# Performance work log

Hardware: AMD Instinct MI355X
Metric: run time of the kernel (lower is better)

## Reference

```python
import jax, jax.numpy as jnp
import numpy as np

NT = 128
T = 262144


def setup_inputs() -> dict:
    key = jax.random.key(0)
    k1, k2, k3, k4, k5 = jax.random.split(key, 5)
    emit = jax.random.normal(k1, (T, NT), dtype=jnp.float32)
    y = jax.random.randint(k2, (T,), 0, NT, dtype=jnp.int64)
    trans = jax.random.normal(k3, (NT, NT), dtype=jnp.float32)
    strans = jax.random.normal(k4, (NT,), dtype=jnp.float32)
    etrans = jax.random.normal(k5, (NT,), dtype=jnp.float32)
    return {"emit": emit, "y": y, "trans": trans, "strans": strans, "etrans": etrans}


def _crf_nll(emit, y, trans, strans, etrans):
    Tlen = emit.shape[0]

    # forward algorithm (log partition) via scan over timesteps 1..T-1
    alpha0 = strans + emit[0]  # [nt]

    def step(alpha, e_t):
        # alpha_new[n] = logsumexp_p(alpha[p] + trans[p, n]) + emit_t[n]
        alpha_new = jax.nn.logsumexp(alpha[:, None] + trans, axis=0) + e_t
        return alpha_new, None

    alpha, _ = jax.lax.scan(step, alpha0, emit[1:])
    logZ = jax.nn.logsumexp(alpha + etrans)

    # gold score (faithful to original: emissions indexed by the *previous* tag)
    prev = y[:-1]
    nxt = y[1:]
    score = strans[y[0]]
    score = score + jnp.sum(trans[prev, nxt] + emit[jnp.arange(Tlen - 1), prev])
    score = score + etrans[y[-1]] + emit[-1, y[-1]]

    return logZ - score


def reference(emit, y, trans, strans, etrans):
    return _crf_nll(emit, y, trans, strans, etrans)
```

## Files before the change

kernel.cpp:

```cpp
#include <hip/hip_runtime.h>

typedef _Float16 f16x4 __attribute__((ext_vector_type(4)));
typedef float    f32x4 __attribute__((ext_vector_type(4)));

#define T_LEN   262144
#define NTAG    128
#define LCH     64
#define BURN    32
#define NSTEP   96
#define MCH     16
#define NFWD    256
#define NSCORE  256

__global__ __launch_bounds__(256) void crf_fused(
    const float* __restrict__ emit, const int* __restrict__ y,
    const float* __restrict__ trans, const float* __restrict__ strans,
    const float* __restrict__ etrans, double* __restrict__ ws)
{
  if (blockIdx.x >= NFWD) {
    __shared__ float sred[4];
    int idx0 = (blockIdx.x - NFWD) * 256 + threadIdx.x;
    float v = 0.f;
    for (int t = idx0; t < T_LEN - 1; t += NSCORE * 256) {
      int yt = y[t], yn = y[t + 1];
      v += trans[yt * NTAG + yn] + emit[(size_t)t * NTAG + yt];
    }
    if (idx0 == 0) {
      int yl = y[T_LEN - 1];
      v += strans[y[0]] + etrans[yl] + emit[(size_t)(T_LEN - 1) * NTAG + yl];
    }
#pragma unroll
    for (int off = 1; off < 64; off <<= 1) v += __shfl_xor(v, off, 64);
    if ((threadIdx.x & 63) == 0) sred[threadIdx.x >> 6] = v;
    __syncthreads();
    if (threadIdx.x == 0)
      atomicAdd(&ws[1], (double)(sred[0] + sred[1] + sred[2] + sred[3]));
    return;
  }

  __shared__ uint2 pb[8][64];
  __shared__ float emlds[MCH][132];
  __shared__ float wmaxT[MCH][4];

  const int tid   = threadIdx.x;
  const int w     = tid >> 6;
  const int l     = tid & 63;
  const int chunk = l & 15;
  const int grp   = l >> 4;
  const int g0    = blockIdx.x * MCH;
  const int gc    = g0 + chunk;
  const bool lane_g0 = (gc == 0);

  f16x4 qa[2][8];
#pragma unroll
  for (int mt = 0; mt < 2; ++mt) {
    const int out = 32 * w + 16 * mt + chunk;
#pragma unroll
    for (int kt = 0; kt < 8; ++kt) {
      f16x4 a;
#pragma unroll
      for (int j = 0; j < 4; ++j)
        a[j] = (_Float16)__expf(trans[(size_t)(16 * kt + 4 * grp + j) * NTAG + out]);
      qa[mt][kt] = a;
    }
  }

  const int c_row = tid >> 4;
  const int c16   = tid & 15;
  auto erow = [&](int i) -> int {
    int gcr = g0 + c_row;
    return (gcr == 0) ? (i + 1) : (gcr * LCH - BURN + i);
  };

  {
    const float* rp = emit + (size_t)erow(0) * NTAG;
    float4 e0 = *(const float4*)(rp + 4 * c16);
    float4 e1 = *(const float4*)(rp + 4 * c16 + 64);
    *(float4*)&emlds[c_row][4 * c16]      = e0;
    *(float4*)&emlds[c_row][4 * c16 + 64] = e1;
  }

  float b[2][4];
#pragma unroll
  for (int mt = 0; mt < 2; ++mt)
#pragma unroll
    for (int r = 0; r < 4; ++r) b[mt][r] = 0.f;
  if (lane_g0) {
#pragma unroll
    for (int mt = 0; mt < 2; ++mt)
#pragma unroll
      for (int r = 0; r < 4; ++r) {
        int tag = 32 * w + 16 * mt + 4 * grp + r;
        b[mt][r] = strans[tag] + emit[tag];
      }
  }
  float vm = b[0][0];
#pragma unroll
  for (int r = 1; r < 4; ++r) vm = fmaxf(vm, b[0][r]);
#pragma unroll
  for (int r = 0; r < 4; ++r) vm = fmaxf(vm, b[1][r]);
  vm = fmaxf(vm, __shfl_xor(vm, 16, 64));
  vm = fmaxf(vm, __shfl_xor(vm, 32, 64));
  if (grp == 0) wmaxT[chunk][w] = vm;
  __syncthreads();
  float4 wm0 = *(const float4*)&wmaxT[chunk][0];
  float m = fmaxf(fmaxf(wm0.x, wm0.y), fmaxf(wm0.z, wm0.w));
  float acc = lane_g0 ? m : 0.f;
#pragma unroll
  for (int mt = 0; mt < 2; ++mt) {
    union { uint2 u; f16x4 h; } pk;
#pragma unroll
    for (int r = 0; r < 4; ++r) pk.h[r] = (_Float16)__expf(b[mt][r] - m);
    pb[2 * w + mt][l] = pk.u;
  }
  __syncthreads();

  float4 pf0, pf1;
  for (int s = 0; s < NSTEP; ++s) {
    if (s < NSTEP - 1) {
      const float* rp = emit + (size_t)erow(s + 1) * NTAG;
      pf0 = *(const float4*)(rp + 4 * c16);
      pf1 = *(const float4*)(rp + 4 * c16 + 64);
    }
    f32x4 c0 = {0.f, 0.f, 0.f, 0.f};
    f32x4 c1 = {0.f, 0.f, 0.f, 0.f};
#pragma unroll
    for (int kt = 0; kt < 8; ++kt) {
      union { uint2 u; f16x4 h; } bf;
      bf.u = pb[kt][l];
      c0 = __builtin_amdgcn_mfma_f32_16x16x16f16(qa[0][kt], bf.h, c0, 0, 0, 0);
      c1 = __builtin_amdgcn_mfma_f32_16x16x16f16(qa[1][kt], bf.h, c1, 0, 0, 0);
    }
    float4 em0 = *(const float4*)&emlds[chunk][32 * w + 4 * grp];
    float4 em1 = *(const float4*)&emlds[chunk][32 * w + 16 + 4 * grp];
    b[0][0] = __logf(c0[0]) + em0.x;
    b[0][1] = __logf(c0[1]) + em0.y;
    b[0][2] = __logf(c0[2]) + em0.z;
    b[0][3] = __logf(c0[3]) + em0.w;
    b[1][0] = __logf(c1[0]) + em1.x;
    b[1][1] = __logf(c1[1]) + em1.y;
    b[1][2] = __logf(c1[2]) + em1.z;
    b[1][3] = __logf(c1[3]) + em1.w;
    vm = b[0][0];
#pragma unroll
    for (int r = 1; r < 4; ++r) vm = fmaxf(vm, b[0][r]);
#pragma unroll
    for (int r = 0; r < 4; ++r) vm = fmaxf(vm, b[1][r]);
    vm = fmaxf(vm, __shfl_xor(vm, 16, 64));
    vm = fmaxf(vm, __shfl_xor(vm, 32, 64));
    if (grp == 0) wmaxT[chunk][w] = vm;
    __syncthreads();
    float4 wm = *(const float4*)&wmaxT[chunk][0];
    m = fmaxf(fmaxf(wm.x, wm.y), fmaxf(wm.z, wm.w));
    {
      int tstate = lane_g0 ? (s + 1) : (gc * LCH - BURN + s);
      if (tstate >= gc * LCH && tstate < gc * LCH + LCH) acc += m;
    }
    float pf[2][4];
#pragma unroll
    for (int mt = 0; mt < 2; ++mt) {
      union { uint2 u; f16x4 h; } pk;
#pragma unroll
      for (int r = 0; r < 4; ++r) {
        pf[mt][r] = __expf(b[mt][r] - m);
        pk.h[r]   = (_Float16)pf[mt][r];
      }
      pb[2 * w + mt][l] = pk.u;
    }
    if (s == NSTEP - 1 && blockIdx.x == NFWD - 1 && chunk == 15) {
      float lv = 0.f;
#pragma unroll
      for (int mt = 0; mt < 2; ++mt)
#pragma unroll
        for (int r = 0; r < 4; ++r)
          lv += pf[mt][r] * __expf(etrans[32 * w + 16 * mt + 4 * grp + r]);
      atomicAdd(&ws[2], (double)lv);
    }
    if (s < NSTEP - 1) {
      *(float4*)&emlds[c_row][4 * c16]      = pf0;
      *(float4*)&emlds[c_row][4 * c16 + 64] = pf1;
    }
    __syncthreads();
  }

  if (w == 0) {
    float a = acc;
#pragma unroll
    for (int off = 1; off < 16; off <<= 1) a += __shfl_xor(a, off, 64);
    if (l == 0) atomicAdd(&ws[0], (double)a);
  }
}

__global__ void crf_final(const double* __restrict__ ws, float* __restrict__ out)
{
  out[0] = (float)(ws[0] + log(ws[2]) - ws[1]);
}

extern "C" void kernel_launch(void* const* d_in, const int* in_sizes, int n_in,
                              void* d_out, int out_size, void* d_ws, size_t ws_size,
                              hipStream_t stream)
{
  const float* emit   = (const float*)d_in[0];
  const int*   y      = (const int*)d_in[1];
  const float* trans  = (const float*)d_in[2];
  const float* strans = (const float*)d_in[3];
  const float* etrans = (const float*)d_in[4];
  float*  out = (float*)d_out;
  double* ws  = (double*)d_ws;

  hipMemsetAsync(ws, 0, 3 * sizeof(double), stream);
  crf_fused<<<dim3(NFWD + NSCORE), dim3(256), 0, stream>>>(
      emit, y, trans, strans, etrans, ws);
  crf_final<<<dim3(1), dim3(1), 0, stream>>>(ws, out);
}
```

Before: 88.60 us.

## Rewrite forward pass as per-wave chunks with full-tag MFMA and in-kernel finalize

Restructures the chunked forward algorithm so each wave owns 16 chunks and computes all 128 output tags itself with a 8x8 MFMA tile held in registers. It removes the LDS exchange and block-wide barriers of the old per-step loop. Chunks shrink to 16 steps with a 16-step burn-in, so there are many more chunks and blocks. The log/exp is replaced by a scaled-probability recurrence that multiplies by exp(emit) and renormalizes by the max. The final combine now runs via a last-block atomic counter instead of a separate kernel. The trade-offs are much higher register pressure from 64 f16x4 A fragments, double the burn-in overhead ratio, and a shorter warm-up that could affect accuracy.

```diff
diff --git a/kernel.cpp b/kernel.cpp
--- a/kernel.cpp
+++ b/kernel.cpp
@@ -5,23 +5,26 @@
 
 #define T_LEN   262144
 #define NTAG    128
-#define LCH     64
-#define BURN    32
-#define NSTEP   96
-#define MCH     16
-#define NFWD    256
-#define NSCORE  256
+#define LCH     16
+#define BURN    16
+#define NSTEP   (LCH + BURN)
+#define NCHUNK  (T_LEN / LCH)
+#define NWAVE   (NCHUNK / 16)
+#define NSCOREB 256
+#define NFWDB   (NWAVE / 4)
+#define NBLK    (NSCOREB + NFWDB)
 
-__global__ __launch_bounds__(256) void crf_fused(
+__global__ __launch_bounds__(256, 2) void crf_all(
     const float* __restrict__ emit, const int* __restrict__ y,
     const float* __restrict__ trans, const float* __restrict__ strans,
-    const float* __restrict__ etrans, double* __restrict__ ws)
+    const float* __restrict__ etrans, double* __restrict__ ws,
+    float* __restrict__ out)
 {
-  if (blockIdx.x >= NFWD) {
+  if (blockIdx.x < NSCOREB) {
     __shared__ float sred[4];
-    int idx0 = (blockIdx.x - NFWD) * 256 + threadIdx.x;
+    int idx0 = blockIdx.x * 256 + threadIdx.x;
     float v = 0.f;
-    for (int t = idx0; t < T_LEN - 1; t += NSCORE * 256) {
+    for (int t = idx0; t < T_LEN - 1; t += NSCOREB * 256) {
       int yt = y[t], yn = y[t + 1];
       v += trans[yt * NTAG + yn] + emit[(size_t)t * NTAG + yt];
     }
@@ -35,165 +38,146 @@
     __syncthreads();
     if (threadIdx.x == 0)
       atomicAdd(&ws[1], (double)(sred[0] + sred[1] + sred[2] + sred[3]));
-    return;
+  } else {
+    const int w   = threadIdx.x >> 6;
+    const int l   = threadIdx.x & 63;
+    const int col = l & 15;
+    const int grp = l >> 4;
+    const int gw  = (blockIdx.x - NSCOREB) * 4 + w;
+    const int gc  = gw * 16 + col;
+
+    f16x4 a[8][8];
+#pragma unroll
+    for (int rt = 0; rt < 8; ++rt) {
+      const int outtag = 16 * rt + col;
+#pragma unroll
+      for (int kt = 0; kt < 8; ++kt) {
+        f16x4 t4;
+#pragma unroll
+        for (int j = 0; j < 4; ++j)
+          t4[j] = (_Float16)__expf(trans[(16 * kt + 4 * grp + j) * NTAG + outtag]);
+        a[rt][kt] = t4;
+      }
+    }
+
+    f16x4 b[8];
+    float acc = 0.f;
+    if (gc == 0) {
+      float al[8][4];
+      float vm = -1e30f;
+#pragma unroll
+      for (int kt = 0; kt < 8; ++kt)
+#pragma unroll
+        for (int r = 0; r < 4; ++r) {
+          int tag = 16 * kt + 4 * grp + r;
+          al[kt][r] = strans[tag] + emit[tag];
+          vm = fmaxf(vm, al[kt][r]);
+        }
+      vm = fmaxf(vm, __shfl_xor(vm, 16, 64));
+      vm = fmaxf(vm, __shfl_xor(vm, 32, 64));
+      acc = vm;
+#pragma unroll
+      for (int kt = 0; kt < 8; ++kt) {
+        f16x4 nb;
+#pragma unroll
+        for (int r = 0; r < 4; ++r) nb[r] = (_Float16)__expf(al[kt][r] - vm);
+        b[kt] = nb;
+      }
+    } else {
+#pragma unroll
+      for (int kt = 0; kt < 8; ++kt) {
+        f16x4 nb;
+#pragma unroll
+        for (int r = 0; r < 4; ++r) nb[r] = (_Float16)1.0f;
+        b[kt] = nb;
+      }
+    }
+
+    const int row0 = (gc == 0) ? 1 : (gc * LCH - BURN);
+    const float* ebase = emit + (size_t)row0 * NTAG + 4 * grp;
+    float4 pf[8];
+#pragma unroll
+    for (int rt = 0; rt < 8; ++rt) pf[rt] = *(const float4*)(ebase + 16 * rt);
+    ebase += NTAG;
+
+#pragma unroll 1
+    for (int s = 0; s < NSTEP; ++s) {
+      f32x4 c[8];
+#pragma unroll
+      for (int rt = 0; rt < 8; ++rt) c[rt] = (f32x4){0.f, 0.f, 0.f, 0.f};
+#pragma unroll
+      for (int kt = 0; kt < 8; ++kt)
+#pragma unroll
+        for (int rt = 0; rt < 8; ++rt)
+          c[rt] = __builtin_amdgcn_mfma_f32_16x16x16f16(a[rt][kt], b[kt], c[rt], 0, 0, 0);
+
+      float e[8][4];
+#pragma unroll
+      for (int rt = 0; rt < 8; ++rt) {
+        e[rt][0] = __expf(pf[rt].x);
+        e[rt][1] = __expf(pf[rt].y);
+        e[rt][2] = __expf(pf[rt].z);
+        e[rt][3] = __expf(pf[rt].w);
+      }
+      if (s < NSTEP - 1) {
+#pragma unroll
+        for (int rt = 0; rt < 8; ++rt) pf[rt] = *(const float4*)(ebase + 16 * rt);
+        ebase += NTAG;
+      }
+
+      float u[8][4];
+      float vm = -1e30f;
+#pragma unroll
+      for (int rt = 0; rt < 8; ++rt)
+#pragma unroll
+        for (int r = 0; r < 4; ++r) {
+          u[rt][r] = c[rt][r] * e[rt][r];
+          vm = fmaxf(vm, u[rt][r]);
+        }
+      vm = fmaxf(vm, __shfl_xor(vm, 16, 64));
+      vm = fmaxf(vm, __shfl_xor(vm, 32, 64));
+      const float lm   = __logf(vm);
+      const bool  on   = (gc == 0) ? (s <= LCH - 2) : (s >= BURN);
+      if (on) acc += lm;
+      const float rinv = __frcp_rn(vm);
+#pragma unroll
+      for (int kt = 0; kt < 8; ++kt) {
+        f16x4 nb;
+#pragma unroll
+        for (int r = 0; r < 4; ++r) nb[r] = (_Float16)(u[kt][r] * rinv);
+        b[kt] = nb;
+      }
+
+      if (s == NSTEP - 1 && gc == NCHUNK - 1) {
+        float lv = 0.f;
+#pragma unroll
+        for (int rt = 0; rt < 8; ++rt)
+#pragma unroll
+          for (int r = 0; r < 4; ++r)
+            lv += (u[rt][r] * rinv) * __expf(etrans[16 * rt + 4 * grp + r]);
+        lv += __shfl_xor(lv, 16, 64);
+        lv += __shfl_xor(lv, 32, 64);
+        if (grp == 0) atomicAdd(&ws[2], (double)lv);
+      }
+    }
+
+    float av = (grp == 0) ? acc : 0.f;
+#pragma unroll
+    for (int off = 1; off < 64; off <<= 1) av += __shfl_xor(av, off, 64);
+    if (l == 0) atomicAdd(&ws[0], (double)av);
   }
 
-  __shared__ uint2 pb[8][64];
-  __shared__ float emlds[MCH][132];
-  __shared__ float wmaxT[MCH][4];
-
-  const int tid   = threadIdx.x;
-  const int w     = tid >> 6;
-  const int l     = tid & 63;
-  const int chunk = l & 15;
-  const int grp   = l >> 4;
-  const int g0    = blockIdx.x * MCH;
-  const int gc    = g0 + chunk;
-  const bool lane_g0 = (gc == 0);
-
-  f16x4 qa[2][8];
-#pragma unroll
-  for (int mt = 0; mt < 2; ++mt) {
-    const int out = 32 * w + 16 * mt + chunk;
-#pragma unroll
-    for (int kt = 0; kt < 8; ++kt) {
-      f16x4 a;
-#pragma unroll
-      for (int j = 0; j < 4; ++j)
-        a[j] = (_Float16)__expf(trans[(size_t)(16 * kt + 4 * grp + j) * NTAG + out]);
-      qa[mt][kt] = a;
+  __syncthreads();
+  if (threadIdx.x == 0) {
+    __threadfence();
+    unsigned t = atomicAdd((unsigned*)&ws[3], 1u);
+    if (t == NBLK - 1) {
+      double d0 = atomicAdd(&ws[0], 0.0);
+      double d1 = atomicAdd(&ws[1], 0.0);
+      double d2 = atomicAdd(&ws[2], 0.0);
+      out[0] = (float)(d0 + log(d2) - d1);
     }
   }
-
-  const int c_row = tid >> 4;
-  const int c16   = tid & 15;
-  auto erow = [&](int i) -> int {
-    int gcr = g0 + c_row;
-    return (gcr == 0) ? (i + 1) : (gcr * LCH - BURN + i);
-  };
-
-  {
-    const float* rp = emit + (size_t)erow(0) * NTAG;
-    float4 e0 = *(const float4*)(rp + 4 * c16);
-    float4 e1 = *(const float4*)(rp + 4 * c16 + 64);
-    *(float4*)&emlds[c_row][4 * c16]      = e0;
-    *(float4*)&emlds[c_row][4 * c16 + 64] = e1;
-  }
-
-  float b[2][4];
-#pragma unroll
-  for (int mt = 0; mt < 2; ++mt)
-#pragma unroll
-    for (int r = 0; r < 4; ++r) b[mt][r] = 0.f;
-  if (lane_g0) {
-#pragma unroll
-    for (int mt = 0; mt < 2; ++mt)
-#pragma unroll
-      for (int r = 0; r < 4; ++r) {
-        int tag = 32 * w + 16 * mt + 4 * grp + r;
-        b[mt][r] = strans[tag] + emit[tag];
-      }
-  }
-  float vm = b[0][0];
-#pragma unroll
-  for (int r = 1; r < 4; ++r) vm = fmaxf(vm, b[0][r]);
-#pragma unroll
-  for (int r = 0; r < 4; ++r) vm = fmaxf(vm, b[1][r]);
-  vm = fmaxf(vm, __shfl_xor(vm, 16, 64));
-  vm = fmaxf(vm, __shfl_xor(vm, 32, 64));
-  if (grp == 0) wmaxT[chunk][w] = vm;
-  __syncthreads();
-  float4 wm0 = *(const float4*)&wmaxT[chunk][0];
-  float m = fmaxf(fmaxf(wm0.x, wm0.y), fmaxf(wm0.z, wm0.w));
-  float acc = lane_g0 ? m : 0.f;
-#pragma unroll
-  for (int mt = 0; mt < 2; ++mt) {
-    union { uint2 u; f16x4 h; } pk;
-#pragma unroll
-    for (int r = 0; r < 4; ++r) pk.h[r] = (_Float16)__expf(b[mt][r] - m);
-    pb[2 * w + mt][l] = pk.u;
-  }
-  __syncthreads();
-
-  float4 pf0, pf1;
-  for (int s = 0; s < NSTEP; ++s) {
-    if (s < NSTEP - 1) {
-      const float* rp = emit + (size_t)erow(s + 1) * NTAG;
-      pf0 = *(const float4*)(rp + 4 * c16);
-      pf1 = *(const float4*)(rp + 4 * c16 + 64);
-    }
-    f32x4 c0 = {0.f, 0.f, 0.f, 0.f};
-    f32x4 c1 = {0.f, 0.f, 0.f, 0.f};
-#pragma unroll
-    for (int kt = 0; kt < 8; ++kt) {
-      union { uint2 u; f16x4 h; } bf;
-      bf.u = pb[kt][l];
-      c0 = __builtin_amdgcn_mfma_f32_16x16x16f16(qa[0][kt], bf.h, c0, 0, 0, 0);
-      c1 = __builtin_amdgcn_mfma_f32_16x16x16f16(qa[1][kt], bf.h, c1, 0, 0, 0);
-    }
-    float4 em0 = *(const float4*)&emlds[chunk][32 * w + 4 * grp];
-    float4 em1 = *(const float4*)&emlds[chunk][32 * w + 16 + 4 * grp];
-    b[0][0] = __logf(c0[0]) + em0.x;
-    b[0][1] = __logf(c0[1]) + em0.y;
-    b[0][2] = __logf(c0[2]) + em0.z;
-    b[0][3] = __logf(c0[3]) + em0.w;
-    b[1][0] = __logf(c1[0]) + em1.x;
-    b[1][1] = __logf(c1[1]) + em1.y;
-    b[1][2] = __logf(c1[2]) + em1.z;
-    b[1][3] = __logf(c1[3]) + em1.w;
-    vm = b[0][0];
-#pragma unroll
-    for (int r = 1; r < 4; ++r) vm = fmaxf(vm, b[0][r]);
-#pragma unroll
-    for (int r = 0; r < 4; ++r) vm = fmaxf(vm, b[1][r]);
-    vm = fmaxf(vm, __shfl_xor(vm, 16, 64));
-    vm = fmaxf(vm, __shfl_xor(vm, 32, 64));
-    if (grp == 0) wmaxT[chunk][w] = vm;
-    __syncthreads();
-    float4 wm = *(const float4*)&wmaxT[chunk][0];
-    m = fmaxf(fmaxf(wm.x, wm.y), fmaxf(wm.z, wm.w));
-    {
-      int tstate = lane_g0 ? (s + 1) : (gc * LCH - BURN + s);
-      if (tstate >= gc * LCH && tstate < gc * LCH + LCH) acc += m;
-    }
-    float pf[2][4];
-#pragma unroll
-    for (int mt = 0; mt < 2; ++mt) {
-      union { uint2 u; f16x4 h; } pk;
-#pragma unroll
-      for (int r = 0; r < 4; ++r) {
-        pf[mt][r] = __expf(b[mt][r] - m);
-        pk.h[r]   = (_Float16)pf[mt][r];
-      }
-      pb[2 * w + mt][l] = pk.u;
-    }
-    if (s == NSTEP - 1 && blockIdx.x == NFWD - 1 && chunk == 15) {
-      float lv = 0.f;
-#pragma unroll
-      for (int mt = 0; mt < 2; ++mt)
-#pragma unroll
-        for (int r = 0; r < 4; ++r)
-          lv += pf[mt][r] * __expf(etrans[32 * w + 16 * mt + 4 * grp + r]);
-      atomicAdd(&ws[2], (double)lv);
-    }
-    if (s < NSTEP - 1) {
-      *(float4*)&emlds[c_row][4 * c16]      = pf0;
-      *(float4*)&emlds[c_row][4 * c16 + 64] = pf1;
-    }
-    __syncthreads();
-  }
-
-  if (w == 0) {
-    float a = acc;
-#pragma unroll
-    for (int off = 1; off < 16; off <<= 1) a += __shfl_xor(a, off, 64);
-    if (l == 0) atomicAdd(&ws[0], (double)a);
-  }
-}
-
-__global__ void crf_final(const double* __restrict__ ws, float* __restrict__ out)
-{
-  out[0] = (float)(ws[0] + log(ws[2]) - ws[1]);
 }
 
 extern "C" void kernel_launch(void* const* d_in, const int* in_sizes, int n_in,
@@ -208,8 +192,7 @@
   float*  out = (float*)d_out;
   double* ws  = (double*)d_ws;
 
-  hipMemsetAsync(ws, 0, 3 * sizeof(double), stream);
-  crf_fused<<<dim3(NFWD + NSCORE), dim3(256), 0, stream>>>(
-      emit, y, trans, strans, etrans, ws);
-  crf_final<<<dim3(1), dim3(1), 0, stream>>>(ws, out);
+  hipMemsetAsync(ws, 0, 4 * sizeof(double), stream);
+  crf_all<<<dim3(NBLK), dim3(256), 0, stream>>>(
+      emit, y, trans, strans, etrans, ws, out);
 }
```

Result: slower. 95.96 us (+8.3%).
